# Performance work log

Measured on AMD Instinct MI355X. Metric: run time of the kernel, lower is better.

The kernel has to match this reference:

```python
import jax, jax.numpy as jnp
import numpy as np

N = 100000
E = 1600000
IN_C, HID_C, OUT_C = 128, 128, 64


def setup_inputs() -> dict:
    key = jax.random.key(0)
    k1, k2, k3, k4, k5, k6 = jax.random.split(key, 6)
    x = jax.random.normal(k1, (N, IN_C), dtype=jnp.float32)
    edge_index = jax.random.randint(k2, (2, E), 0, N, dtype=jnp.int64)
    # Glorot-style init like PyG GCNConv Linear
    W1 = jax.random.normal(k3, (IN_C, HID_C), dtype=jnp.float32) / np.sqrt(IN_C)
    b1 = jnp.zeros((HID_C,), dtype=jnp.float32)
    W2 = jax.random.normal(k4, (HID_C, OUT_C), dtype=jnp.float32) / np.sqrt(HID_C)
    b2 = jnp.zeros((OUT_C,), dtype=jnp.float32)
    return {"x": x, "edge_index": edge_index, "W1": W1, "b1": b1, "W2": W2, "b2": b2}


def gcn_conv(x, src, dst, norm, W, b, n_nodes):
    # x: [N, F_in]; src/dst/norm: [E+N] (self-loops included)
    h = x @ W                                   # [N, F_out] small GEMM
    msg = h[src] * norm[:, None]                # [E+N, F_out] gather (dominant)
    out = jax.ops.segment_sum(msg, dst, num_segments=n_nodes)  # scatter-add
    return out + b


def gcn_norm(edge_index, n_nodes):
    # add self-loops, then symmetric normalization D^-1/2 (A+I) D^-1/2
    loop = jnp.arange(n_nodes, dtype=edge_index.dtype)
    src = jnp.concatenate([edge_index[0], loop])
    dst = jnp.concatenate([edge_index[1], loop])
    deg = jax.ops.segment_sum(jnp.ones_like(dst, dtype=jnp.float32), dst,
                              num_segments=n_nodes)
    dinv = jnp.where(deg > 0, jax.lax.rsqrt(jnp.maximum(deg, 1.0)), 0.0)
    norm = dinv[src] * dinv[dst]
    return src, dst, norm


def reference(x, edge_index, W1, b1, W2, b2):
    n_nodes = x.shape[0]
    src, dst, norm = gcn_norm(edge_index, n_nodes)  # cached=True -> computed once
    h = gcn_conv(x, src, dst, norm, W1, b1, n_nodes)
    h = jax.nn.relu(h)
    # dropout in eval mode (training=False) is identity
    out = gcn_conv(h, src, dst, norm, W2, b2, n_nodes)
    return out
```

## Files before the change

### kernel.cpp

```cpp
#include <hip/hip_runtime.h>
#include <hip/hip_fp16.h>

constexpr int NN  = 100000;
constexpr int NE  = 1600000;
constexpr int TOT = NE + NN;

constexpr int NBUK    = (NN + 255) / 256;
constexpr int EBLOCKS = 512;
constexpr int EPB     = NE / EBLOCKS;

typedef _Float16 f16x8 __attribute__((ext_vector_type(8)));
typedef float    f32x4 __attribute__((ext_vector_type(4)));

__device__ inline float2 h2f2(unsigned int u) {
  __half2 h = __builtin_bit_cast(__half2, u);
  return __half22float2(h);
}
__device__ inline unsigned int f2h2(float a, float b) {
  __half2 h = __floats2half2_rn(a, b);
  return __builtin_bit_cast(unsigned int, h);
}

__device__ inline int block_is64(const unsigned int* ei) {
  unsigned int w = ei[threadIdx.x * 2 + 1];
  int nz = __syncthreads_count(w != 0u);
  return nz == 0;
}

__device__ inline int load_idx(const void* ei, long long i, int is64) {
  return is64 ? (int)((const long long*)ei)[i] : ((const int*)ei)[i];
}


__global__ __launch_bounds__(256) void k_hist(const void* __restrict__ ei, int* __restrict__ hist_g) {
  __shared__ int h[NBUK];
  int is64 = block_is64((const unsigned int*)ei);
  for (int i = threadIdx.x; i < NBUK; i += 256) h[i] = 0;
  __syncthreads();
  int e0 = blockIdx.x * EPB;
  for (int e = e0 + threadIdx.x; e < e0 + EPB; e += 256) {
    int d = load_idx(ei, (long long)NE + e, is64);
    atomicAdd(&h[d >> 8], 1);
  }
  __syncthreads();
  for (int i = threadIdx.x; i < NBUK; i += 256)
    hist_g[i * EBLOCKS + blockIdx.x] = h[i];
}

__global__ __launch_bounds__(512) void k_scan_hist(int* __restrict__ hist_g, int* __restrict__ bucket_total) {
  __shared__ int s[EBLOCKS];
  int b = blockIdx.x, t = threadIdx.x;
  int v = hist_g[b * EBLOCKS + t];
  s[t] = v;
  __syncthreads();
  for (int off = 1; off < EBLOCKS; off <<= 1) {
    int u = (t >= off) ? s[t - off] : 0;
    __syncthreads();
    s[t] += u;
    __syncthreads();
  }
  hist_g[b * EBLOCKS + t] = s[t] - v;
  if (t == EBLOCKS - 1) bucket_total[b] = s[t];
}

__global__ __launch_bounds__(512) void k_scan_buckets(const int* __restrict__ bucket_total,
                                                      int* __restrict__ edge_base, int* __restrict__ row_start) {
  __shared__ int s[512];
  int t = threadIdx.x;
  int v = (t < NBUK) ? bucket_total[t] : 0;
  s[t] = v;
  __syncthreads();
  for (int off = 1; off < 512; off <<= 1) {
    int u = (t >= off) ? s[t - off] : 0;
    __syncthreads();
    s[t] += u;
    __syncthreads();
  }
  if (t <= NBUK) edge_base[t] = s[t] - v;
  if (t == 0) row_start[NN] = TOT;
}

__global__ __launch_bounds__(256) void k_scatter(const void* __restrict__ ei,
                                                 const int* __restrict__ hist_g, const int* __restrict__ edge_base,
                                                 int* __restrict__ rec) {
  __shared__ int cur[NBUK];
  int is64 = block_is64((const unsigned int*)ei);
  for (int i = threadIdx.x; i < NBUK; i += 256)
    cur[i] = edge_base[i] + hist_g[i * EBLOCKS + blockIdx.x];
  __syncthreads();
  int e0 = blockIdx.x * EPB;
  for (int e = e0 + threadIdx.x; e < e0 + EPB; e += 256) {
    int sA = load_idx(ei, e, is64);
    int d  = load_idx(ei, (long long)NE + e, is64);
    int p = atomicAdd(&cur[d >> 8], 1);
    rec[p] = (sA << 8) | (d & 255);
  }
}

__global__ __launch_bounds__(256) void k_bucket_csr(const int* __restrict__ rec, const int* __restrict__ edge_base,
                                                    int* __restrict__ row_start, float* __restrict__ dinv,
                                                    int* __restrict__ csr_src) {
  __shared__ int cnt[256];
  __shared__ int s[256];
  int b = blockIdx.x, t = threadIdx.x;
  int node = b * 256 + t;
  cnt[t] = 0;
  __syncthreads();
  int j0 = edge_base[b], j1 = edge_base[b + 1];
  for (int j = j0 + t; j < j1; j += 256)
    atomicAdd(&cnt[rec[j] & 255], 1);
  __syncthreads();
  int c = (node < NN) ? cnt[t] + 1 : 0;
  s[t] = c;
  __syncthreads();
  for (int off = 1; off < 256; off <<= 1) {
    int u = (t >= off) ? s[t - off] : 0;
    __syncthreads();
    s[t] += u;
    __syncthreads();
  }
  int csr_b = j0 + b * 256;
  int start = csr_b + s[t] - c;
  if (node < NN) {
    row_start[node] = start;
    dinv[node] = rsqrtf((float)c);
    csr_src[start] = node;
  }
  __syncthreads();
  cnt[t] = start + 1;
  __syncthreads();
  for (int j = j0 + t; j < j1; j += 256) {
    int r = rec[j];
    int p = atomicAdd(&cnt[r & 255], 1);
    csr_src[p] = r >> 8;
  }
}

template<int OUTC>
__global__ __launch_bounds__(256) void k_gemm_mfma(const float* __restrict__ X,
                                                   const float* __restrict__ W,
                                                   const float* __restrict__ dinv,
                                                   unsigned short* __restrict__ Y) {
  constexpr int NT = OUTC / 16;
  constexpr int PS = 136;
  constexpr int SS = OUTC + 8;
  constexpr int WT_H = OUTC * PS;
  constexpr int ST_H = 64 * SS;
  constexpr int SM_H = WT_H > ST_H ? WT_H : ST_H;
  __shared__ _Float16 smem[SM_H];

  const int tid  = threadIdx.x;
  const int lane = tid & 63;
  const int wv   = tid >> 6;
  const int row0 = blockIdx.x * 64;
  const int l15  = lane & 15;
  const int kg   = lane >> 4;

  for (int idx = tid * 4; idx < 128 * OUTC; idx += 1024) {
    float4 v = *(const float4*)&W[idx];
    int k = idx / OUTC, c = idx % OUTC;
    smem[(c + 0) * PS + k] = (_Float16)v.x;
    smem[(c + 1) * PS + k] = (_Float16)v.y;
    smem[(c + 2) * PS + k] = (_Float16)v.z;
    smem[(c + 3) * PS + k] = (_Float16)v.w;
  }
  __syncthreads();

  int arow = row0 + wv * 16 + l15;
  int rr_g = arow < NN ? arow : NN - 1;

  f32x4 acc[NT];
  #pragma unroll
  for (int n = 0; n < NT; n++) acc[n] = (f32x4){0.f, 0.f, 0.f, 0.f};

  #pragma unroll
  for (int kb = 0; kb < 4; kb++) {
    int k0 = kb * 32 + kg * 8;
    f16x8 a;
    float4 v0 = *(const float4*)&X[(size_t)rr_g * 128 + k0];
    float4 v1 = *(const float4*)&X[(size_t)rr_g * 128 + k0 + 4];
    a[0] = (_Float16)v0.x; a[1] = (_Float16)v0.y; a[2] = (_Float16)v0.z; a[3] = (_Float16)v0.w;
    a[4] = (_Float16)v1.x; a[5] = (_Float16)v1.y; a[6] = (_Float16)v1.z; a[7] = (_Float16)v1.w;
    #pragma unroll
    for (int n = 0; n < NT; n++) {
      f16x8 b = *(const f16x8*)&smem[(n * 16 + l15) * PS + k0];
      acc[n] = __builtin_amdgcn_mfma_f32_16x16x32_f16(a, b, acc[n], 0, 0, 0);
    }
  }
  __syncthreads();

  int rb = wv * 16 + kg * 4;
  float dv[4];
  #pragma unroll
  for (int q = 0; q < 4; q++) {
    int gr = row0 + rb + q;
    dv[q] = dinv[gr < NN ? gr : NN - 1];
  }
  #pragma unroll
  for (int n = 0; n < NT; n++)
    #pragma unroll
    for (int q = 0; q < 4; q++)
      smem[(rb + q) * SS + n * 16 + l15] = (_Float16)(acc[n][q] * dv[q]);
  __syncthreads();

  constexpr int SEGS = OUTC / 8;
  for (int u = tid; u < 64 * SEGS; u += 256) {
    int rr = u / SEGS, sg = u % SEGS;
    int gr = row0 + rr;
    if (gr < NN) {
      uint4 v = *(const uint4*)&smem[rr * SS + sg * 8];
      *(uint4*)&Y[(size_t)gr * OUTC + sg * 8] = v;
    }
  }
}

__global__ __launch_bounds__(256) void k_agg_gemm(const unsigned short* __restrict__ h,
                                                  const float* __restrict__ dinv,
                                                  const int* __restrict__ row_start,
                                                  const int* __restrict__ csr_src,
                                                  const float* __restrict__ bias,
                                                  const float* __restrict__ W,
                                                  unsigned short* __restrict__ Y) {
  constexpr int PS = 136;
  constexpr int AS = 136;
  constexpr int OS = 72;
  __shared__ _Float16 Wt[64 * PS];
  __shared__ _Float16 At[16 * AS];

  const int tid = threadIdx.x;

  for (int idx = tid * 4; idx < 128 * 64; idx += 1024) {
    float4 v = *(const float4*)&W[idx];
    int k = idx >> 6, c = idx & 63;
    Wt[(c + 0) * PS + k] = (_Float16)v.x;
    Wt[(c + 1) * PS + k] = (_Float16)v.y;
    Wt[(c + 2) * PS + k] = (_Float16)v.z;
    Wt[(c + 3) * PS + k] = (_Float16)v.w;
  }

  const int ln    = tid & 15;
  const int lnode = tid >> 4;
  const int node  = blockIdx.x * 16 + lnode;

  int j0 = row_start[node], j1 = row_start[node + 1];
  float acc[8] = {};
  #pragma unroll 2
  for (int j = j0; j < j1; j++) {
    int s = csr_src[j];
    uint4 v = *(const uint4*)&h[(size_t)s * 128 + ln * 8];
    float2 f;
    f = h2f2(v.x); acc[0] += f.x; acc[1] += f.y;
    f = h2f2(v.y); acc[2] += f.x; acc[3] += f.y;
    f = h2f2(v.z); acc[4] += f.x; acc[5] += f.y;
    f = h2f2(v.w); acc[6] += f.x; acc[7] += f.y;
  }
  float dn = dinv[node];
  #pragma unroll
  for (int t = 0; t < 8; t++) {
    float o = fmaf(dn, acc[t], bias[ln * 8 + t]);
    o = fmaxf(o, 0.f);
    At[lnode * AS + ln * 8 + t] = (_Float16)o;
  }
  __syncthreads();

  const int lane = tid & 63;
  const int wv   = tid >> 6;
  const int l15  = lane & 15;
  const int kg   = lane >> 4;
  f32x4 dacc = (f32x4){0.f, 0.f, 0.f, 0.f};
  #pragma unroll
  for (int kb = 0; kb < 4; kb++) {
    int k0 = kb * 32 + kg * 8;
    f16x8 a = *(const f16x8*)&At[l15 * AS + k0];
    f16x8 b = *(const f16x8*)&Wt[(wv * 16 + l15) * PS + k0];
    dacc = __builtin_amdgcn_mfma_f32_16x16x32_f16(a, b, dacc, 0, 0, 0);
  }
  __syncthreads();

  #pragma unroll
  for (int q = 0; q < 4; q++) {
    int lr = kg * 4 + q;
    float dv = dinv[blockIdx.x * 16 + lr];
    At[lr * OS + wv * 16 + l15] = (_Float16)(dacc[q] * dv);
  }
  __syncthreads();

  for (int u = tid; u < 16 * 8; u += 256) {
    int rr = u >> 3, sg = u & 7;
    uint4 v = *(const uint4*)&At[rr * OS + sg * 8];
    *(uint4*)&Y[(size_t)(blockIdx.x * 16 + rr) * 64 + sg * 8] = v;
  }
}

__global__ __launch_bounds__(256) void k_agg_final(const unsigned short* __restrict__ h,
                                                   const float* __restrict__ dinv,
                                                   const int* __restrict__ row_start,
                                                   const int* __restrict__ csr_src,
                                                   const float* __restrict__ bias,
                                                   float* __restrict__ out) {
  constexpr int LPN = 8;
  int node = blockIdx.x * 32 + threadIdx.x / LPN;
  int lane = threadIdx.x % LPN;
  if (node >= NN) return;
  int j0 = row_start[node], j1 = row_start[node + 1];
  float acc[8] = {};
  #pragma unroll 2
  for (int j = j0; j < j1; j++) {
    int s = csr_src[j];
    uint4 v = *(const uint4*)&h[(size_t)s * 64 + lane * 8];
    float2 f;
    f = h2f2(v.x); acc[0] += f.x; acc[1] += f.y;
    f = h2f2(v.y); acc[2] += f.x; acc[3] += f.y;
    f = h2f2(v.z); acc[4] += f.x; acc[5] += f.y;
    f = h2f2(v.w); acc[6] += f.x; acc[7] += f.y;
  }
  float dn = dinv[node];
  float o[8];
  #pragma unroll
  for (int t = 0; t < 8; t++) o[t] = fmaf(dn, acc[t], bias[lane * 8 + t]);
  *(float4*)&out[(size_t)node * 64 + lane * 8]     = make_float4(o[0], o[1], o[2], o[3]);
  *(float4*)&out[(size_t)node * 64 + lane * 8 + 4] = make_float4(o[4], o[5], o[6], o[7]);
}

extern "C" void kernel_launch(void* const* d_in, const int* in_sizes, int n_in,
                              void* d_out, int out_size, void* d_ws, size_t ws_size,
                              hipStream_t stream) {
  const float* x  = (const float*)d_in[0];
  const void*  ei = d_in[1];
  const float* W1 = (const float*)d_in[2];
  const float* b1 = (const float*)d_in[3];
  const float* W2 = (const float*)d_in[4];
  const float* b2 = (const float*)d_in[5];
  float* out = (float*)d_out;

  char* ws = (char*)d_ws;
  size_t off = 0;
  auto wsalloc = [&](size_t bytes) -> void* {
    void* p = ws + off;
    off += (bytes + 255) & ~(size_t)255;
    return p;
  };
  int*            row_start    = (int*)   wsalloc((NN + 1) * sizeof(int));
  int*            hist_g       = (int*)   wsalloc((size_t)NBUK * EBLOCKS * sizeof(int));
  int*            bucket_total = (int*)   wsalloc(NBUK * sizeof(int));
  int*            edge_base    = (int*)   wsalloc((NBUK + 1) * sizeof(int));
  float*          dinv         = (float*) wsalloc(NN * sizeof(float));
  int*            rec          = (int*)   wsalloc((size_t)NE * sizeof(int));
  int*            csr_src      = (int*)   wsalloc((size_t)TOT * sizeof(int));
  unsigned short* h1           = (unsigned short*)wsalloc((size_t)NN * 128 * sizeof(unsigned short));
  unsigned short* hL2          = (unsigned short*)wsalloc((size_t)NN * 64 * sizeof(unsigned short));

  k_hist<<<EBLOCKS, 256, 0, stream>>>(ei, hist_g);
  k_scan_hist<<<NBUK, EBLOCKS, 0, stream>>>(hist_g, bucket_total);
  k_scan_buckets<<<1, 512, 0, stream>>>(bucket_total, edge_base, row_start);
  k_scatter<<<EBLOCKS, 256, 0, stream>>>(ei, hist_g, edge_base, rec);
  k_bucket_csr<<<NBUK, 256, 0, stream>>>(rec, edge_base, row_start, dinv, csr_src);

  k_gemm_mfma<128><<<(NN + 63) / 64, 256, 0, stream>>>(x, W1, dinv, h1);
  k_agg_gemm<<<NN / 16, 256, 0, stream>>>(h1, dinv, row_start, csr_src, b1, W2, hL2);
  k_agg_final<<<(NN + 31) / 32, 256, 0, stream>>>(hL2, dinv, row_start, csr_src, b2, out);
}
```

Before: 278.0 us.

## Process 64 nodes per block in fused aggregate-GEMM and transpose W conflict-free

The fused layer-1 aggregation plus layer-2 GEMM kernel now handles 64 nodes per block instead of 16. That spreads the per-block staging of W2 into shared memory over four times as many rows and gives each wave four MFMA tiles per shared B fragment. The W transpose into shared memory, in both GEMM kernels, now uses coalesced column reads and one 4-wide half-precision store per thread instead of scattered scalar stores. The trade-off is fewer blocks and larger shared memory per block, which may reduce occupancy and latency hiding in the gather loop.

```diff
diff --git a/kernel.cpp b/kernel.cpp
--- a/kernel.cpp
+++ b/kernel.cpp
@@ -10,6 +10,7 @@
 constexpr int EPB     = NE / EBLOCKS;
 
 typedef _Float16 f16x8 __attribute__((ext_vector_type(8)));
+typedef _Float16 f16x4 __attribute__((ext_vector_type(4)));
 typedef float    f32x4 __attribute__((ext_vector_type(4)));
 
 __device__ inline float2 h2f2(unsigned int u) {
@@ -156,13 +157,18 @@
   const int l15  = lane & 15;
   const int kg   = lane >> 4;
 
-  for (int idx = tid * 4; idx < 128 * OUTC; idx += 1024) {
-    float4 v = *(const float4*)&W[idx];
-    int k = idx / OUTC, c = idx % OUTC;
-    smem[(c + 0) * PS + k] = (_Float16)v.x;
-    smem[(c + 1) * PS + k] = (_Float16)v.y;
-    smem[(c + 2) * PS + k] = (_Float16)v.z;
-    smem[(c + 3) * PS + k] = (_Float16)v.w;
+  {
+    int c  = tid & (OUTC - 1);
+    int k4 = tid / OUTC;
+    for (int kk = k4; kk < 32; kk += 256 / OUTC) {
+      int k = kk * 4;
+      f16x4 w;
+      w[0] = (_Float16)W[(k + 0) * OUTC + c];
+      w[1] = (_Float16)W[(k + 1) * OUTC + c];
+      w[2] = (_Float16)W[(k + 2) * OUTC + c];
+      w[3] = (_Float16)W[(k + 3) * OUTC + c];
+      *(f16x4*)&smem[c * PS + k] = w;
+    }
   }
   __syncthreads();
 
@@ -225,41 +231,57 @@
   constexpr int AS = 136;
   constexpr int OS = 72;
   __shared__ _Float16 Wt[64 * PS];
-  __shared__ _Float16 At[16 * AS];
-
-  const int tid = threadIdx.x;
-
-  for (int idx = tid * 4; idx < 128 * 64; idx += 1024) {
-    float4 v = *(const float4*)&W[idx];
-    int k = idx >> 6, c = idx & 63;
-    Wt[(c + 0) * PS + k] = (_Float16)v.x;
-    Wt[(c + 1) * PS + k] = (_Float16)v.y;
-    Wt[(c + 2) * PS + k] = (_Float16)v.z;
-    Wt[(c + 3) * PS + k] = (_Float16)v.w;
-  }
-
-  const int ln    = tid & 15;
-  const int lnode = tid >> 4;
-  const int node  = blockIdx.x * 16 + lnode;
-
-  int j0 = row_start[node], j1 = row_start[node + 1];
-  float acc[8] = {};
-  #pragma unroll 2
-  for (int j = j0; j < j1; j++) {
-    int s = csr_src[j];
-    uint4 v = *(const uint4*)&h[(size_t)s * 128 + ln * 8];
-    float2 f;
-    f = h2f2(v.x); acc[0] += f.x; acc[1] += f.y;
-    f = h2f2(v.y); acc[2] += f.x; acc[3] += f.y;
-    f = h2f2(v.z); acc[4] += f.x; acc[5] += f.y;
-    f = h2f2(v.w); acc[6] += f.x; acc[7] += f.y;
-  }
-  float dn = dinv[node];
-  #pragma unroll
-  for (int t = 0; t < 8; t++) {
-    float o = fmaf(dn, acc[t], bias[ln * 8 + t]);
-    o = fmaxf(o, 0.f);
-    At[lnode * AS + ln * 8 + t] = (_Float16)o;
+  __shared__ _Float16 At[64 * AS];
+
+  const int tid  = threadIdx.x;
+  const int row0 = blockIdx.x * 64;
+
+  {
+    int c  = tid & 63;
+    int k4 = tid >> 6;
+    for (int kk = k4; kk < 32; kk += 4) {
+      int k = kk * 4;
+      f16x4 w;
+      w[0] = (_Float16)W[(k + 0) * 64 + c];
+      w[1] = (_Float16)W[(k + 1) * 64 + c];
+      w[2] = (_Float16)W[(k + 2) * 64 + c];
+      w[3] = (_Float16)W[(k + 3) * 64 + c];
+      *(f16x4*)&Wt[c * PS + k] = w;
+    }
+  }
+
+  const int ln  = tid & 15;
+  const int lno = tid >> 4;
+  #pragma unroll
+  for (int g = 0; g < 4; g++) {
+    int lnode = g * 16 + lno;
+    int node  = row0 + lnode;
+    int nc    = node < NN ? node : NN - 1;
+    int j0 = row_start[nc], j1 = row_start[nc + 1];
+    float acc[8] = {};
+    #pragma unroll 2
+    for (int j = j0; j < j1; j++) {
+      int s = csr_src[j];
+      uint4 v = *(const uint4*)&h[(size_t)s * 128 + ln * 8];
+      float2 f;
+      f = h2f2(v.x); acc[0] += f.x; acc[1] += f.y;
+      f = h2f2(v.y); acc[2] += f.x; acc[3] += f.y;
+      f = h2f2(v.z); acc[4] += f.x; acc[5] += f.y;
+      f = h2f2(v.w); acc[6] += f.x; acc[7] += f.y;
+    }
+    float dn = dinv[nc];
+    float o[8];
+    #pragma unroll
+    for (int t = 0; t < 8; t++) {
+      o[t] = fmaf(dn, acc[t], bias[ln * 8 + t]);
+      o[t] = fmaxf(o[t], 0.f);
+    }
+    uint4 pk;
+    pk.x = f2h2(o[0], o[1]);
+    pk.y = f2h2(o[2], o[3]);
+    pk.z = f2h2(o[4], o[5]);
+    pk.w = f2h2(o[6], o[7]);
+    *(uint4*)&At[lnode * AS + ln * 8] = pk;
   }
   __syncthreads();
 
@@ -267,28 +289,39 @@
   const int wv   = tid >> 6;
   const int l15  = lane & 15;
   const int kg   = lane >> 4;
-  f32x4 dacc = (f32x4){0.f, 0.f, 0.f, 0.f};
+  f32x4 dacc[4];
+  #pragma unroll
+  for (int m = 0; m < 4; m++) dacc[m] = (f32x4){0.f, 0.f, 0.f, 0.f};
   #pragma unroll
   for (int kb = 0; kb < 4; kb++) {
     int k0 = kb * 32 + kg * 8;
-    f16x8 a = *(const f16x8*)&At[l15 * AS + k0];
     f16x8 b = *(const f16x8*)&Wt[(wv * 16 + l15) * PS + k0];
-    dacc = __builtin_amdgcn_mfma_f32_16x16x32_f16(a, b, dacc, 0, 0, 0);
-  }
-  __syncthreads();
-
-  #pragma unroll
-  for (int q = 0; q < 4; q++) {
-    int lr = kg * 4 + q;
-    float dv = dinv[blockIdx.x * 16 + lr];
-    At[lr * OS + wv * 16 + l15] = (_Float16)(dacc[q] * dv);
-  }
-  __syncthreads();
-
-  for (int u = tid; u < 16 * 8; u += 256) {
+    #pragma unroll
+    for (int m = 0; m < 4; m++) {
+      f16x8 a = *(const f16x8*)&At[(m * 16 + l15) * AS + k0];
+      dacc[m] = __builtin_amdgcn_mfma_f32_16x16x32_f16(a, b, dacc[m], 0, 0, 0);
+    }
+  }
+  __syncthreads();
+
+  #pragma unroll
+  for (int m = 0; m < 4; m++)
+    #pragma unroll
+    for (int q = 0; q < 4; q++) {
+      int lr = m * 16 + kg * 4 + q;
+      int gr = row0 + lr;
+      float dv = dinv[gr < NN ? gr : NN - 1];
+      At[lr * OS + wv * 16 + l15] = (_Float16)(dacc[m][q] * dv);
+    }
+  __syncthreads();
+
+  for (int u = tid; u < 64 * 8; u += 256) {
     int rr = u >> 3, sg = u & 7;
-    uint4 v = *(const uint4*)&At[rr * OS + sg * 8];
-    *(uint4*)&Y[(size_t)(blockIdx.x * 16 + rr) * 64 + sg * 8] = v;
+    int gr = row0 + rr;
+    if (gr < NN) {
+      uint4 v = *(const uint4*)&At[rr * OS + sg * 8];
+      *(uint4*)&Y[(size_t)gr * 64 + sg * 8] = v;
+    }
   }
 }
 
@@ -357,6 +390,6 @@
   k_bucket_csr<<<NBUK, 256, 0, stream>>>(rec, edge_base, row_start, dinv, csr_src);
 
   k_gemm_mfma<128><<<(NN + 63) / 64, 256, 0, stream>>>(x, W1, dinv, h1);
-  k_agg_gemm<<<NN / 16, 256, 0, stream>>>(h1, dinv, row_start, csr_src, b1, W2, hL2);
+  k_agg_gemm<<<(NN + 63) / 64, 256, 0, stream>>>(h1, dinv, row_start, csr_src, b1, W2, hL2);
   k_agg_final<<<(NN + 31) / 32, 256, 0, stream>>>(hL2, dinv, row_start, csr_src, b2, out);
 }
```

Result: slower. 284.1 us (+2.2%).
